# Kernel tuning notes

Hardware: AMD Instinct MI355X
Metric: run time of the kernel (lower is better)

The kernel has to match this reference:

```python
import jax, jax.numpy as jnp
import numpy as np

INPUT_SIZE = 2048
REDUCED = 128
HIDDEN = 32


def setup_inputs() -> dict:
    key = jax.random.key(0)
    ks = jax.random.split(key, 12)
    N, T, S = 32, 1024, 8
    x = jax.random.normal(ks[0], (N, S, 768), dtype=jnp.float32)
    fea = jax.random.normal(ks[1], (N, T, INPUT_SIZE), dtype=jnp.float32)
    fea_len = jax.random.randint(ks[2], (N,), 0, T - S).astype(jnp.int64)
    s_ann = 1.0 / np.sqrt(INPUT_SIZE)
    s_rnn = 1.0 / np.sqrt(HIDDEN)
    s_q = 1.0 / np.sqrt(HIDDEN)
    W_ann = jax.random.uniform(ks[3], (REDUCED, INPUT_SIZE), minval=-s_ann, maxval=s_ann)
    b_ann = jax.random.uniform(ks[4], (REDUCED,), minval=-s_ann, maxval=s_ann)
    W_ih = jax.random.uniform(ks[5], (3 * HIDDEN, REDUCED), minval=-s_rnn, maxval=s_rnn)
    W_hh = jax.random.uniform(ks[6], (3 * HIDDEN, HIDDEN), minval=-s_rnn, maxval=s_rnn)
    b_ih = jax.random.uniform(ks[7], (3 * HIDDEN,), minval=-s_rnn, maxval=s_rnn)
    b_hh = jax.random.uniform(ks[8], (3 * HIDDEN,), minval=-s_rnn, maxval=s_rnn)
    W_q = jax.random.uniform(ks[9], (1, HIDDEN), minval=-s_q, maxval=s_q)
    b_q = jax.random.uniform(ks[10], (1,), minval=-s_q, maxval=s_q)
    return {"x": x, "fea": fea, "fea_len": fea_len, "W_ann": W_ann, "b_ann": b_ann,
            "W_ih": W_ih, "W_hh": W_hh, "b_ih": b_ih, "b_hh": b_hh,
            "W_q": W_q, "b_q": b_q}


def _gru(gx, W_hh, b_hh, h0):
    # gx: (T, N, 3H) precomputed input projections; torch gate order: r, z, n
    def step(h, gxt):
        gh = h @ W_hh.T + b_hh
        xr, xz, xn = jnp.split(gxt, 3, axis=-1)
        hr, hz, hn = jnp.split(gh, 3, axis=-1)
        r = jax.nn.sigmoid(xr + hr)
        z = jax.nn.sigmoid(xz + hz)
        n = jnp.tanh(xn + r * hn)
        h_new = (1.0 - z) * n + z * h
        return h_new, h_new
    _, hs = jax.lax.scan(step, h0, gx)
    return hs  # (T, N, H)


def reference(x, fea, fea_len, W_ann, b_ann, W_ih, W_hh, b_ih, b_hh, W_q, b_q):
    N, T, _ = fea.shape
    f = fea @ W_ann.T + b_ann                    # (N, T, 128)
    gx = f @ W_ih.T + b_ih                       # (N, T, 3H)
    h0 = jnp.zeros((N, HIDDEN), dtype=f.dtype)
    hs = _gru(jnp.swapaxes(gx, 0, 1), W_hh, b_hh, h0)   # (T, N, H)
    outputs = jnp.swapaxes(hs, 0, 1)             # (N, T, H)
    q = (outputs @ W_q.T + b_q)[..., 0]          # (N, T)
    # vectorized masked segment-mean replacing the per-sample python loop
    L = fea_len + x.shape[1]                     # (N,)
    mask = jnp.arange(T)[None, :] < L[:, None]   # (N, T)
    score = jnp.sum(q * mask, axis=1) / L.astype(q.dtype)
    return score
```

## Files before the change

kernel.cpp:

```cpp
#include <hip/hip_runtime.h>
#include <hip/hip_bf16.h>
#include <math.h>

#define NS   32
#define TS   1024
#define KIN  2048
#define RED  128
#define HID  32
#define G3   96
#define SEQ  8

#define GX_FLOATS (NS * TS * G3)
#define W_ELEMS   (G3 * KIN)

typedef __attribute__((ext_vector_type(8))) short  short8;
typedef __attribute__((ext_vector_type(4))) float  floatx4;

__device__ __forceinline__ int load_len(const int* __restrict__ p, int n) {
    bool is64 = (p[1] == 0) && (p[3] == 0) && (p[5] == 0) && (p[7] == 0);
    if (is64) return (int)((const long long*)p)[n];
    return p[n];
}

__device__ __forceinline__ float fsig(float x) {
    return 1.0f / (1.0f + __expf(-x));
}
__device__ __forceinline__ float ftanh(float x) {
    float ax = fabsf(x);
    float e  = __expf(-2.0f * ax);
    float r  = (1.0f - e) / (1.0f + e);
    return copysignf(r, x);
}

__device__ __forceinline__ unsigned short f2bf(float x) {
    unsigned u = __float_as_uint(x);
    unsigned r = u + 0x7fffu + ((u >> 16) & 1u);
    return (unsigned short)(r >> 16);
}
__device__ __forceinline__ float bfu2f(unsigned short u) {
    return __uint_as_float(((unsigned)u) << 16);
}

__device__ __forceinline__ void cvt_hilo(const float* f, short8& hi, short8& lo) {
    #pragma unroll
    for (int p = 0; p < 4; ++p) {
        float2 fv = make_float2(f[2*p], f[2*p+1]);
        union { __hip_bfloat162 b2; unsigned short us[2]; } H, L;
        H.b2 = __float22bfloat162_rn(fv);
        float2 hb = __bfloat1622float2(H.b2);
        L.b2 = __float22bfloat162_rn(make_float2(fv.x - hb.x, fv.y - hb.y));
        hi[2*p] = (short)H.us[0]; hi[2*p+1] = (short)H.us[1];
        lo[2*p] = (short)L.us[0]; lo[2*p+1] = (short)L.us[1];
    }
}

__global__ __launch_bounds__(256) void k_prep(
        const float* __restrict__ W_ann, const float* __restrict__ b_ann,
        const float* __restrict__ W_ih,  const float* __restrict__ b_ih,
        unsigned short* __restrict__ Whi, unsigned short* __restrict__ Wlo,
        float* __restrict__ b_comb) {
    if (blockIdx.x == 768) {
        int j = threadIdx.x;
        if (j < G3) {
            float acc = b_ih[j];
            #pragma unroll 8
            for (int m = 0; m < RED; ++m) acc += W_ih[j * RED + m] * b_ann[m];
            b_comb[j] = acc;
        }
        return;
    }
    int id = blockIdx.x * 256 + threadIdx.x;
    int j = id >> 11;
    int k = id & (KIN - 1);
    float acc = 0.0f;
    #pragma unroll 8
    for (int m = 0; m < RED; ++m) acc += W_ih[j * RED + m] * W_ann[m * KIN + k];
    unsigned short h = f2bf(acc);
    Whi[id] = h;
    Wlo[id] = f2bf(acc - bfu2f(h));
}

__global__ __launch_bounds__(256) void k_gemm(
        const float* __restrict__ fea, const int* __restrict__ flen,
        const unsigned short* __restrict__ Whi,
        const unsigned short* __restrict__ Wlo,
        const float* __restrict__ b_comb,
        float* __restrict__ gx) {
    const int n  = blockIdx.x;
    const int t0 = blockIdx.y * 128;
    const int L  = load_len(flen, n) + SEQ;
    if (t0 >= L) return;

    const int tid  = threadIdx.x;
    const int w    = tid >> 6;
    const int ln   = tid & 63;
    const int mr   = ln & 15;
    const int quad = ln >> 4;

    const size_t arow0 = ((size_t)(n * TS + t0 + w * 32 + mr)) * KIN + quad * 8;
    const size_t arow1 = arow0 + (size_t)16 * KIN;
    int boff[6];
    #pragma unroll
    for (int nf = 0; nf < 6; ++nf) boff[nf] = (nf * 16 + mr) * KIN + quad * 8;

    floatx4 acc[2][6];
    #pragma unroll
    for (int mf = 0; mf < 2; ++mf)
        #pragma unroll
        for (int nf = 0; nf < 6; ++nf) acc[mf][nf] = (floatx4){0.f, 0.f, 0.f, 0.f};

    #pragma unroll 1
    for (int c = 0; c < KIN / 64; ++c) {
        #pragma unroll
        for (int ks = 0; ks < 2; ++ks) {
            const int ko = c * 64 + ks * 32;
            float fa[8], fb[8];
            {
                float4 a0 = *(const float4*)(fea + arow0 + ko);
                float4 a1 = *(const float4*)(fea + arow0 + ko + 4);
                float4 b0 = *(const float4*)(fea + arow1 + ko);
                float4 b1 = *(const float4*)(fea + arow1 + ko + 4);
                fa[0]=a0.x; fa[1]=a0.y; fa[2]=a0.z; fa[3]=a0.w;
                fa[4]=a1.x; fa[5]=a1.y; fa[6]=a1.z; fa[7]=a1.w;
                fb[0]=b0.x; fb[1]=b0.y; fb[2]=b0.z; fb[3]=b0.w;
                fb[4]=b1.x; fb[5]=b1.y; fb[6]=b1.z; fb[7]=b1.w;
            }
            short8 ah0, al0, ah1, al1;
            cvt_hilo(fa, ah0, al0);
            cvt_hilo(fb, ah1, al1);
            #pragma unroll
            for (int nf = 0; nf < 6; ++nf) {
                short8 bh = *(const short8*)(Whi + boff[nf] + ko);
                short8 bl = *(const short8*)(Wlo + boff[nf] + ko);
                acc[0][nf] = __builtin_amdgcn_mfma_f32_16x16x32_bf16(ah0, bh, acc[0][nf], 0, 0, 0);
                acc[0][nf] = __builtin_amdgcn_mfma_f32_16x16x32_bf16(ah0, bl, acc[0][nf], 0, 0, 0);
                acc[0][nf] = __builtin_amdgcn_mfma_f32_16x16x32_bf16(al0, bh, acc[0][nf], 0, 0, 0);
                acc[1][nf] = __builtin_amdgcn_mfma_f32_16x16x32_bf16(ah1, bh, acc[1][nf], 0, 0, 0);
                acc[1][nf] = __builtin_amdgcn_mfma_f32_16x16x32_bf16(ah1, bl, acc[1][nf], 0, 0, 0);
                acc[1][nf] = __builtin_amdgcn_mfma_f32_16x16x32_bf16(al1, bh, acc[1][nf], 0, 0, 0);
            }
        }
    }

    #pragma unroll
    for (int mf = 0; mf < 2; ++mf) {
        const int tbase = t0 + w * 32 + mf * 16 + quad * 4;
        #pragma unroll
        for (int nf = 0; nf < 6; ++nf) {
            const float bc = b_comb[nf * 16 + mr];
            float* gp = gx + ((size_t)(n * TS + tbase)) * G3 + nf * 16 + mr;
            #pragma unroll
            for (int r = 0; r < 4; ++r)
                gp[(size_t)r * G3] = acc[mf][nf][r] + bc;
        }
    }
}

__global__ __launch_bounds__(64) void k_scan(
        const float* __restrict__ gx, const int* __restrict__ flen,
        const float* __restrict__ W_hh, const float* __restrict__ b_hh,
        const float* __restrict__ W_q,  const float* __restrict__ b_q,
        float* __restrict__ out) {
    const int n    = blockIdx.x;
    const int lane = threadIdx.x;
    const int j    = lane & 31;
    const int kh   = lane >> 5;
    const int L    = load_len(flen, n) + SEQ;
    const int sbase = kh << 4;

    float wr[16], wz[16], wn[16];
    {
        const float4* Wr4 = (const float4*)(W_hh + (size_t)(j)      * HID + sbase);
        const float4* Wz4 = (const float4*)(W_hh + (size_t)(32 + j) * HID + sbase);
        const float4* Wn4 = (const float4*)(W_hh + (size_t)(64 + j) * HID + sbase);
        #pragma unroll
        for (int p = 0; p < 4; ++p) {
            float4 v;
            v = Wr4[p]; wr[4*p] = v.x; wr[4*p+1] = v.y; wr[4*p+2] = v.z; wr[4*p+3] = v.w;
            v = Wz4[p]; wz[4*p] = v.x; wz[4*p+1] = v.y; wz[4*p+2] = v.z; wz[4*p+3] = v.w;
            v = Wn4[p]; wn[4*p] = v.x; wn[4*p+1] = v.y; wn[4*p+2] = v.z; wn[4*p+3] = v.w;
        }
    }
    const float br = b_hh[j], bz = b_hh[32 + j], bn = b_hh[64 + j];
    const float wq = W_q[j];
    const float bq = b_q[0];

    const float* gbase = gx + (size_t)n * TS * G3;
    const bool xon = (kh == 0);

    float rg[8][3];
    #pragma unroll
    for (int i = 0; i < 8; ++i) {
        const float* p = gbase + (size_t)i * G3;
        rg[i][0] = p[j]; rg[i][1] = p[32 + j]; rg[i][2] = p[64 + j];
    }

    float hv[16];
    #pragma unroll
    for (int i = 0; i < 16; ++i) hv[i] = 0.0f;
    float h = 0.0f, qacc = 0.0f;

    for (int tb = 0; tb < L; tb += 8) {
        #pragma unroll
        for (int i = 0; i < 8; ++i) {
            const int t = tb + i;
            float xr = xon ? rg[i][0] : 0.0f;
            float xz = xon ? rg[i][1] : 0.0f;
            float xn = xon ? rg[i][2] : 0.0f;
            {
                int tl = t + 8; if (tl > TS - 1) tl = TS - 1;
                const float* p = gbase + (size_t)tl * G3;
                rg[i][0] = p[j]; rg[i][1] = p[32 + j]; rg[i][2] = p[64 + j];
            }

            float gr0 = 0.f, gr1 = 0.f, gz0 = 0.f, gz1 = 0.f, gn0 = 0.f, gn1 = 0.f;
            #pragma unroll
            for (int q2 = 0; q2 < 16; q2 += 2) {
                gr0 += wr[q2] * hv[q2];     gr1 += wr[q2+1] * hv[q2+1];
                gz0 += wz[q2] * hv[q2];     gz1 += wz[q2+1] * hv[q2+1];
                gn0 += wn[q2] * hv[q2];     gn1 += wn[q2+1] * hv[q2+1];
            }
            float c0 = xr + gr0 + gr1;
            float c1 = xz + gz0 + gz1;
            float c2 = gn0 + gn1;
            float c3 = xn;
            c0 += __shfl_xor(c0, 32, 64);
            c1 += __shfl_xor(c1, 32, 64);
            c2 += __shfl_xor(c2, 32, 64);
            c3 += __shfl_xor(c3, 32, 64);

            float r    = fsig(c0 + br);
            float z    = fsig(c1 + bz);
            float nng  = ftanh(c3 + r * (c2 + bn));
            float hnew = (1.0f - z) * nng + z * h;
            if (t < L) {
                h = hnew;
                qacc += wq * hnew;
            }

            #pragma unroll
            for (int q2 = 0; q2 < 16; ++q2) hv[q2] = __shfl(h, sbase + q2, 64);
        }
    }

    #pragma unroll
    for (int off = 32; off > 0; off >>= 1) qacc += __shfl_xor(qacc, off, 64);
    if (lane == 0) out[n] = qacc * 0.5f / (float)L + bq;
}

extern "C" void kernel_launch(void* const* d_in, const int* in_sizes, int n_in,
                              void* d_out, int out_size, void* d_ws, size_t ws_size,
                              hipStream_t stream) {
    const float* fea   = (const float*)d_in[1];
    const int*   flen  = (const int*)  d_in[2];
    const float* W_ann = (const float*)d_in[3];
    const float* b_ann = (const float*)d_in[4];
    const float* W_ih  = (const float*)d_in[5];
    const float* W_hh  = (const float*)d_in[6];
    const float* b_ih  = (const float*)d_in[7];
    const float* b_hh  = (const float*)d_in[8];
    const float* W_q   = (const float*)d_in[9];
    const float* b_q   = (const float*)d_in[10];
    float* out = (float*)d_out;

    float*          ws_f   = (float*)d_ws;
    float*          gx     = ws_f;
    unsigned short* Whi    = (unsigned short*)(ws_f + GX_FLOATS);
    unsigned short* Wlo    = Whi + W_ELEMS;
    float*          b_comb = (float*)(Wlo + W_ELEMS);

    k_prep<<<769, 256, 0, stream>>>(W_ann, b_ann, W_ih, b_ih, Whi, Wlo, b_comb);

    dim3 g2(NS, TS / 128);
    k_gemm<<<g2, 256, 0, stream>>>(fea, flen, Whi, Wlo, b_comb, gx);

    k_scan<<<NS, 64, 0, stream>>>(gx, flen, W_hh, b_hh, W_q, b_q, out);
}
```

Measured before the change: 762.7 us.

## Replace scan shuffles with permlane swaps and DPP broadcasts, pack FMAs

Inside the sequential GRU scan kernel, the 16 per-step ds_bpermute shuffles that broadcast h are replaced with one permlane16 swap and a tree of DPP row moves. The W_hh weights are permuted to match the lane order those moves produce. The cross-half reduction now uses permlane32 swaps instead of xor shuffles, the dot products use packed float2 math, and the divides become rcp approximations. This shortens the latency-bound dependency chain per timestep, at the cost of a fragile lane-mapping permutation and less exact sigmoid and tanh.

```diff
diff --git a/kernel.cpp b/kernel.cpp
--- a/kernel.cpp
+++ b/kernel.cpp
@@ -15,6 +15,8 @@
 
 typedef __attribute__((ext_vector_type(8))) short  short8;
 typedef __attribute__((ext_vector_type(4))) float  floatx4;
+typedef __attribute__((ext_vector_type(2))) float  floatx2;
+typedef __attribute__((ext_vector_type(2))) unsigned int uint2v;
 
 __device__ __forceinline__ int load_len(const int* __restrict__ p, int n) {
     bool is64 = (p[1] == 0) && (p[3] == 0) && (p[5] == 0) && (p[7] == 0);
@@ -23,12 +25,12 @@
 }
 
 __device__ __forceinline__ float fsig(float x) {
-    return 1.0f / (1.0f + __expf(-x));
+    return __builtin_amdgcn_rcpf(1.0f + __expf(-x));
 }
 __device__ __forceinline__ float ftanh(float x) {
     float ax = fabsf(x);
     float e  = __expf(-2.0f * ax);
-    float r  = (1.0f - e) / (1.0f + e);
+    float r  = (1.0f - e) * __builtin_amdgcn_rcpf(1.0f + e);
     return copysignf(r, x);
 }
 
@@ -40,6 +42,32 @@
 __device__ __forceinline__ float bfu2f(unsigned short u) {
     return __uint_as_float(((unsigned)u) << 16);
 }
+
+__device__ __forceinline__ void swap16(unsigned& a, unsigned& b) {
+#if __has_builtin(__builtin_amdgcn_permlane16_swap)
+    uint2v r = __builtin_amdgcn_permlane16_swap(a, b, false, false);
+    a = r.x; b = r.y;
+#else
+    asm("v_permlane16_swap_b32 %0, %1" : "+v"(a), "+v"(b));
+#endif
+}
+__device__ __forceinline__ void swap32(unsigned& a, unsigned& b) {
+#if __has_builtin(__builtin_amdgcn_permlane32_swap)
+    uint2v r = __builtin_amdgcn_permlane32_swap(a, b, false, false);
+    a = r.x; b = r.y;
+#else
+    asm("v_permlane32_swap_b32 %0, %1" : "+v"(a), "+v"(b));
+#endif
+}
+
+__device__ __forceinline__ float xor32sum(float x) {
+    unsigned a = __float_as_uint(x), b = a;
+    swap32(a, b);
+    return __uint_as_float(a) + __uint_as_float(b);
+}
+
+#define DPPM(srcv, ctrl) __uint_as_float((unsigned)__builtin_amdgcn_update_dpp( \
+        (int)__float_as_uint(srcv), (int)__float_as_uint(srcv), (ctrl), 0xF, 0xF, false))
 
 __device__ __forceinline__ void cvt_hilo(const float* f, short8& hi, short8& lo) {
     #pragma unroll
@@ -156,7 +184,7 @@
     }
 }
 
-__global__ __launch_bounds__(64) void k_scan(
+__global__ __launch_bounds__(64, 1) void k_scan(
         const float* __restrict__ gx, const int* __restrict__ flen,
         const float* __restrict__ W_hh, const float* __restrict__ b_hh,
         const float* __restrict__ W_q,  const float* __restrict__ b_q,
@@ -165,28 +193,37 @@
     const int lane = threadIdx.x;
     const int j    = lane & 31;
     const int kh   = lane >> 5;
+    const int l15  = lane & 15;
     const int L    = load_len(flen, n) + SEQ;
-    const int sbase = kh << 4;
-
-    float wr[16], wz[16], wn[16];
-    {
-        const float4* Wr4 = (const float4*)(W_hh + (size_t)(j)      * HID + sbase);
-        const float4* Wz4 = (const float4*)(W_hh + (size_t)(32 + j) * HID + sbase);
-        const float4* Wn4 = (const float4*)(W_hh + (size_t)(64 + j) * HID + sbase);
-        #pragma unroll
-        for (int p = 0; p < 4; ++p) {
-            float4 v;
-            v = Wr4[p]; wr[4*p] = v.x; wr[4*p+1] = v.y; wr[4*p+2] = v.z; wr[4*p+3] = v.w;
-            v = Wz4[p]; wz[4*p] = v.x; wz[4*p+1] = v.y; wz[4*p+2] = v.z; wz[4*p+3] = v.w;
-            v = Wn4[p]; wn[4*p] = v.x; wn[4*p+1] = v.y; wn[4*p+2] = v.z; wn[4*p+3] = v.w;
-        }
+
+    const int MT[16] = {0,1,2,3, 7,6,5,4, 15,14,13,12, 8,9,10,11};
+
+    floatx2 wr2[8], wz2[8], wn2[8];
+    #pragma unroll
+    for (int k2 = 0; k2 < 8; ++k2) {
+        const int ka = kh * 16 + (l15 ^ MT[2*k2]);
+        const int kb = kh * 16 + (l15 ^ MT[2*k2+1]);
+        wr2[k2].x = W_hh[(size_t)(j)      * HID + ka];
+        wr2[k2].y = W_hh[(size_t)(j)      * HID + kb];
+        wz2[k2].x = W_hh[(size_t)(32 + j) * HID + ka];
+        wz2[k2].y = W_hh[(size_t)(32 + j) * HID + kb];
+        wn2[k2].x = W_hh[(size_t)(64 + j) * HID + ka];
+        wn2[k2].y = W_hh[(size_t)(64 + j) * HID + kb];
     }
     const float br = b_hh[j], bz = b_hh[32 + j], bn = b_hh[64 + j];
     const float wq = W_q[j];
     const float bq = b_q[0];
+    const bool  hi = (lane >= 32);
+
+    bool selY;
+    {
+        unsigned a = (unsigned)lane, b = (unsigned)lane;
+        swap16(a, b);
+        const bool dirA = ((a & 16u) == 0u);
+        selY = dirA ? hi : !hi;
+    }
 
     const float* gbase = gx + (size_t)n * TS * G3;
-    const bool xon = (kh == 0);
 
     float rg[8][3];
     #pragma unroll
@@ -195,51 +232,64 @@
         rg[i][0] = p[j]; rg[i][1] = p[32 + j]; rg[i][2] = p[64 + j];
     }
 
-    float hv[16];
-    #pragma unroll
-    for (int i = 0; i < 16; ++i) hv[i] = 0.0f;
+    floatx2 hv2[8];
+    #pragma unroll
+    for (int k2 = 0; k2 < 8; ++k2) hv2[k2] = (floatx2){0.f, 0.f};
     float h = 0.0f, qacc = 0.0f;
 
     for (int tb = 0; tb < L; tb += 8) {
         #pragma unroll
         for (int i = 0; i < 8; ++i) {
             const int t = tb + i;
-            float xr = xon ? rg[i][0] : 0.0f;
-            float xz = xon ? rg[i][1] : 0.0f;
-            float xn = xon ? rg[i][2] : 0.0f;
+            const float xr = rg[i][0], xz = rg[i][1], xn = rg[i][2];
             {
                 int tl = t + 8; if (tl > TS - 1) tl = TS - 1;
                 const float* p = gbase + (size_t)tl * G3;
                 rg[i][0] = p[j]; rg[i][1] = p[32 + j]; rg[i][2] = p[64 + j];
             }
 
-            float gr0 = 0.f, gr1 = 0.f, gz0 = 0.f, gz1 = 0.f, gn0 = 0.f, gn1 = 0.f;
+            floatx2 ar = (floatx2){0.f, 0.f};
+            floatx2 az = (floatx2){0.f, 0.f};
+            floatx2 an = (floatx2){0.f, 0.f};
             #pragma unroll
-            for (int q2 = 0; q2 < 16; q2 += 2) {
-                gr0 += wr[q2] * hv[q2];     gr1 += wr[q2+1] * hv[q2+1];
-                gz0 += wz[q2] * hv[q2];     gz1 += wz[q2+1] * hv[q2+1];
-                gn0 += wn[q2] * hv[q2];     gn1 += wn[q2+1] * hv[q2+1];
-            }
-            float c0 = xr + gr0 + gr1;
-            float c1 = xz + gz0 + gz1;
-            float c2 = gn0 + gn1;
-            float c3 = xn;
-            c0 += __shfl_xor(c0, 32, 64);
-            c1 += __shfl_xor(c1, 32, 64);
-            c2 += __shfl_xor(c2, 32, 64);
-            c3 += __shfl_xor(c3, 32, 64);
-
-            float r    = fsig(c0 + br);
-            float z    = fsig(c1 + bz);
-            float nng  = ftanh(c3 + r * (c2 + bn));
-            float hnew = (1.0f - z) * nng + z * h;
+            for (int k2 = 0; k2 < 8; ++k2) {
+                ar += wr2[k2] * hv2[k2];
+                az += wz2[k2] * hv2[k2];
+                an += wn2[k2] * hv2[k2];
+            }
+            float dr = xor32sum(ar.x + ar.y);
+            float dz = xor32sum(az.x + az.y);
+            float dn = xor32sum(an.x + an.y);
+
+            float r    = fsig(xr + dr + br);
+            float z    = fsig(xz + dz + bz);
+            float nng  = ftanh(xn + r * (dn + bn));
+            float hnew = nng + z * (h - nng);
             if (t < L) {
                 h = hnew;
                 qacc += wq * hnew;
             }
 
-            #pragma unroll
-            for (int q2 = 0; q2 < 16; ++q2) hv[q2] = __shfl(h, sbase + q2, 64);
+            {
+                unsigned pa = __float_as_uint(h), pb = pa;
+                swap16(pa, pb);
+                hv2[0].x = selY ? __uint_as_float(pb) : __uint_as_float(pa);
+                hv2[0].y = DPPM(hv2[0].x, 0xB1);
+                hv2[1].x = DPPM(hv2[0].x, 0x4E);
+                hv2[1].y = DPPM(hv2[0].y, 0x4E);
+                hv2[2].x = DPPM(hv2[0].x, 0x141);
+                hv2[2].y = DPPM(hv2[0].y, 0x141);
+                hv2[3].x = DPPM(hv2[1].x, 0x141);
+                hv2[3].y = DPPM(hv2[1].y, 0x141);
+                hv2[4].x = DPPM(hv2[0].x, 0x140);
+                hv2[4].y = DPPM(hv2[0].y, 0x140);
+                hv2[5].x = DPPM(hv2[1].x, 0x140);
+                hv2[5].y = DPPM(hv2[1].y, 0x140);
+                hv2[6].x = DPPM(hv2[2].x, 0x140);
+                hv2[6].y = DPPM(hv2[2].y, 0x140);
+                hv2[7].x = DPPM(hv2[3].x, 0x140);
+                hv2[7].y = DPPM(hv2[3].y, 0x140);
+            }
         }
     }
 
```

Measured after the change: 687.6 us. -9.8%, faster.
